# Kernel tuning notes

Measured on AMD Instinct MI355X. Metric: run time of the kernel, lower is better.

Reference implementation:

```python
import jax, jax.numpy as jnp
import numpy as np

N_OUT = 4096
N_IN = 4096
NNZ = 1600000
BATCH = 4096


def setup_inputs() -> dict:
    key = jax.random.key(0)
    k1, k2, k3, k4, k5 = jax.random.split(key, 5)
    inputs = jax.random.normal(k1, (N_IN, BATCH), dtype=jnp.float32)
    values = jax.random.normal(k2, (NNZ,), dtype=jnp.float32)
    biases = jax.random.normal(k3, (N_OUT, 1), dtype=jnp.float32)
    rows = jax.random.randint(k4, (NNZ,), 0, N_OUT, dtype=jnp.int32)
    cols = jax.random.randint(k5, (NNZ,), 0, N_IN, dtype=jnp.int32)
    return {"inputs": inputs, "values": values, "biases": biases,
            "rows": rows, "cols": cols}


def reference(inputs, values, biases, rows, cols):
    # torch.sparse.addmm(biases, W_sparse, inputs) with W COO [N_OUT, N_IN].
    # Scatter-add COO entries into a dense weight (duplicates summed, matching
    # coalesce semantics), then one dense GEMM -- avoids an [NNZ, BATCH]
    # gather intermediate while computing identical math.
    W = jnp.zeros((N_OUT, N_IN), dtype=values.dtype).at[rows, cols].add(values)
    out = W @ inputs + biases  # [N_OUT, BATCH], bias broadcast over columns
    return jax.nn.relu(out)    # activation epilogue
```

## Files before the change

### kernel.cpp

```cpp
#include <hip/hip_runtime.h>
#include <stdint.h>

#define N_OUT_  4096
#define N_IN_   4096
#define BATCH_  4096
#define NNZ_    1600000

typedef unsigned short ushort_t;
typedef float  f32x4  __attribute__((ext_vector_type(4)));
typedef short  short8 __attribute__((ext_vector_type(8)));
typedef __bf16 bf16x8 __attribute__((ext_vector_type(8)));

__device__ inline ushort_t f32_to_bf16(float f) {
  uint32_t u = __float_as_uint(f);
  uint32_t r = u + 0x7FFFu + ((u >> 16) & 1u);
  return (ushort_t)(r >> 16);
}
__device__ inline float bf16_to_f32(ushort_t h) {
  return __uint_as_float(((uint32_t)h) << 16);
}

__device__ inline void gload_lds16(const void* g, void* l) {
  __builtin_amdgcn_global_load_lds(
      (const __attribute__((address_space(1))) void*)g,
      (__attribute__((address_space(3))) void*)l,
      16, 0, 0);
}

__device__ inline f32x4 mfma_bf16(short8 a, short8 b, f32x4 c) {
  return __builtin_amdgcn_mfma_f32_16x16x32_bf16(
      __builtin_bit_cast(bf16x8, a), __builtin_bit_cast(bf16x8, b), c, 0, 0, 0);
}

#define BARRIER() asm volatile("s_barrier" ::: "memory")
template <int N> __device__ __forceinline__ void waitvm() {
  if constexpr (N == 8)      asm volatile("s_waitcnt vmcnt(8)" ::: "memory");
  else if constexpr (N == 6) asm volatile("s_waitcnt vmcnt(6)" ::: "memory");
  else if constexpr (N == 4) asm volatile("s_waitcnt vmcnt(4)" ::: "memory");
  else                       asm volatile("s_waitcnt vmcnt(0)" ::: "memory");
}

#define SC_BLOCKS2 3125
#define TR_TOTAL 4096
#define FUSED_BLOCKS 7294
#define HALF_NNZ 800000

__device__ inline void cas_add_bf16(uint32_t* __restrict__ W32, int i,
                                    const float* __restrict__ vals,
                                    const int* __restrict__ rows,
                                    const int* __restrict__ cols) {
  const size_t idx =
      (size_t)__builtin_nontemporal_load(rows + i) * N_IN_ +
      __builtin_nontemporal_load(cols + i);
  const float v = __builtin_nontemporal_load(vals + i);
  uint32_t* p = &W32[idx >> 1];
  const bool hi = (idx & 1) != 0;
  uint32_t cur = 0u;
  while (true) {
    ushort_t h = hi ? (ushort_t)(cur >> 16) : (ushort_t)(cur & 0xFFFFu);
    ushort_t nh = f32_to_bf16(bf16_to_f32(h) + v);
    uint32_t nw = hi ? ((cur & 0x0000FFFFu) | ((uint32_t)nh << 16))
                     : ((cur & 0xFFFF0000u) | (uint32_t)nh);
    uint32_t got = atomicCAS(p, cur, nw);
    if (got == cur) break;
    cur = got;
  }
}

__global__ __launch_bounds__(256) void scatter_transpose(
    const float* __restrict__ vals, const int* __restrict__ rows,
    const int* __restrict__ cols, uint32_t* __restrict__ W32,
    const float* __restrict__ in, ushort_t* __restrict__ out) {
  const int b = blockIdx.x;
  const int m = b % 7;
  if (m < 3) {
    const int sb = (b / 7) * 3 + m;
    if (sb >= SC_BLOCKS2) return;
    const int i = sb * 256 + threadIdx.x;
    cas_add_bf16(W32, i, vals, rows, cols);
    cas_add_bf16(W32, i + HALF_NNZ, vals, rows, cols);
  } else {
    const int tb = (b / 7) * 4 + (m - 3);
    if (tb >= TR_TOTAL) return;
    __shared__ float tile[64][65];
    const int bx = (tb & 63) * 64;
    const int by = (tb >> 6) * 64;
    const int t = threadIdx.x;
    const int lr = t >> 4;
    const int lc = (t & 15) * 4;
#pragma unroll
    for (int p = 0; p < 4; ++p) {
      const int i = lr + 16 * p;
      *(float4*)&tile[i][lc] =
          *(const float4*)&in[(size_t)(by + i) * BATCH_ + bx + lc];
    }
    __syncthreads();
    const int s = t & 7;
    const int j0 = t >> 3;
#pragma unroll
    for (int q = 0; q < 2; ++q) {
      const int j = j0 + 32 * q;
      uint32_t w0, w1, w2, w3;
      w0 = (uint32_t)f32_to_bf16(tile[8 * s + 0][j]) |
           ((uint32_t)f32_to_bf16(tile[8 * s + 1][j]) << 16);
      w1 = (uint32_t)f32_to_bf16(tile[8 * s + 2][j]) |
           ((uint32_t)f32_to_bf16(tile[8 * s + 3][j]) << 16);
      w2 = (uint32_t)f32_to_bf16(tile[8 * s + 4][j]) |
           ((uint32_t)f32_to_bf16(tile[8 * s + 5][j]) << 16);
      w3 = (uint32_t)f32_to_bf16(tile[8 * s + 6][j]) |
           ((uint32_t)f32_to_bf16(tile[8 * s + 7][j]) << 16);
      uint4 w = {w0, w1, w2, w3};
      *(uint4*)&out[(size_t)(bx + j) * N_IN_ + by + 8 * s] = w;
    }
  }
}

#define BM 256
#define BN 256
#define BK 32
#define KTILES 128
#define TILE_BYTES 32768
#define B_OFF 16384

__global__ __launch_bounds__(512, 2) void gemm_bias_relu(
    const ushort_t* __restrict__ A,
    const ushort_t* __restrict__ Bt,
    const float* __restrict__ bias,
    float* __restrict__ C) {
  __shared__ __align__(16) char smem[4 * TILE_BYTES];

  const int tid  = threadIdx.x;
  const int wid  = tid >> 6;
  const int lane = tid & 63;

  const int bid = blockIdx.x;
  const int swz = (bid & 7) * 32 + (bid >> 3);
  const int brow = (swz >> 4) * BM;
  const int bcol = (swz & 15) * BN;

  const int wr = wid >> 2;
  const int wc = wid & 3;
  const int fr = lane & 15;
  const int k0slot = lane >> 4;

  int aoff[8], boff[4];
#pragma unroll
  for (int mi = 0; mi < 8; ++mi) {
    int off = (wr * 128 + mi * 16 + fr) * 64 + k0slot * 16;
    aoff[mi] = off ^ (((off >> 7) & 3) << 4);
  }
#pragma unroll
  for (int ni = 0; ni < 4; ++ni) {
    int off = (wc * 64 + ni * 16 + fr) * 64 + k0slot * 16;
    boff[ni] = off ^ (((off >> 7) & 3) << 4);
  }

  const bool isB = wid >= 4;
  const int sw = isB ? wid - 4 : wid;
  const int swzl = lane ^ ((lane >> 3) & 3);
  const int rowInChunk = swzl >> 2;
  const int kelem = (swzl & 3) * 8;
  const ushort_t* gsrc = isB ? Bt : A;
  const size_t laneRowBase =
      (size_t)((isB ? bcol : brow) + sw * 64 + rowInChunk) * N_IN_ + kelem;
  const int ldsOpBase = isB ? B_OFF : 0;

#define STAGE(p, i, t)                                                        \
  gload_lds16(gsrc + laneRowBase + (size_t)(2 * (p) + (i)) * 16 * N_IN_ +     \
                  (size_t)(t) * BK,                                           \
              smem + ((t) & 3) * TILE_BYTES + ldsOpBase +                     \
                  (4 * sw + 2 * (p) + (i)) * 1024)

  f32x4 acc[8][4] = {};
  short8 aE[4], bE[4], aO[4], bO[4], aH[4];

#pragma unroll
  for (int t = 0; t < 3; ++t) {
    STAGE(0, 0, t); STAGE(0, 1, t); STAGE(1, 0, t); STAGE(1, 1, t);
  }
  waitvm<8>();
  BARRIER();
#pragma unroll
  for (int j = 0; j < 4; ++j) {
    aE[j] = *(const short8*)(smem + aoff[j]);
    bE[j] = *(const short8*)(smem + B_OFF + boff[j]);
  }

#define TILE(t, AL, BB, ALn, BBn, S_ON, VM, RA_ON)                            \
  do {                                                                        \
    const char* buf  = &smem[((t) & 3) * TILE_BYTES];                         \
    const char* bufn = &smem[(((t) + 1) & 3) * TILE_BYTES];                   \
    _Pragma("unroll") for (int j = 0; j < 4; ++j)                             \
        aH[j] = *(const short8*)(buf + aoff[j + 4]);                          \
    if (S_ON) { STAGE(0, 0, (t) + 3); STAGE(0, 1, (t) + 3); }                 \
    VM;                                                                       \
    BARRIER();                                                                \
    __builtin_amdgcn_s_setprio(1);                                            \
    _Pragma("unroll") for (int mi = 0; mi < 4; ++mi)                          \
        _Pragma("unroll") for (int ni = 0; ni < 4; ++ni)                      \
            acc[mi][ni] = mfma_bf16(AL[mi], BB[ni], acc[mi][ni]);             \
    __builtin_amdgcn_s_setprio(0);                                            \
    if (RA_ON) {                                                              \
      _Pragma("unroll") for (int j = 0; j < 4; ++j)                           \
          ALn[j] = *(const short8*)(bufn + aoff[j]);                          \
      _Pragma("unroll") for (int j = 0; j < 4; ++j)                           \
          BBn[j] = *(const short8*)(bufn + B_OFF + boff[j]);                  \
    }                                                                         \
    if (S_ON) { STAGE(1, 0, (t) + 3); STAGE(1, 1, (t) + 3); }                 \
    __builtin_amdgcn_s_setprio(1);                                            \
    _Pragma("unroll") for (int mi = 0; mi < 4; ++mi)                          \
        _Pragma("unroll") for (int ni = 0; ni < 4; ++ni)                      \
            acc[mi + 4][ni] = mfma_bf16(aH[mi], BB[ni], acc[mi + 4][ni]);     \
    __builtin_amdgcn_s_setprio(0);                                            \
    BARRIER();                                                                \
  } while (0)

  for (int t = 0; t < KTILES - 4; t += 2) {
    TILE(t,     aE, bE, aO, bO, 1, waitvm<6>(), 1);
    TILE(t + 1, aO, bO, aE, bE, 1, waitvm<6>(), 1);
  }
  TILE(KTILES - 4, aE, bE, aO, bO, 1, waitvm<6>(), 1);
  TILE(KTILES - 3, aO, bO, aE, bE, 0, waitvm<4>(), 1);
  TILE(KTILES - 2, aE, bE, aO, bO, 0, waitvm<0>(), 1);
  TILE(KTILES - 1, aO, bO, aE, bE, 0, (void)0,     0);

  const int r0 = brow + wr * 128 + k0slot * 4;
  const int c0 = bcol + wc * 64 + fr;
#pragma unroll
  for (int mi = 0; mi < 8; ++mi) {
#pragma unroll
    for (int r = 0; r < 4; ++r) {
      const int row = r0 + mi * 16 + r;
      const float b = bias[row];
#pragma unroll
      for (int ni = 0; ni < 4; ++ni) {
        float v = acc[mi][ni][r] + b;
        C[(size_t)row * BATCH_ + c0 + ni * 16] = v > 0.f ? v : 0.f;
      }
    }
  }
#undef TILE
#undef STAGE
}

extern "C" void kernel_launch(void* const* d_in, const int* in_sizes, int n_in,
                              void* d_out, int out_size, void* d_ws, size_t ws_size,
                              hipStream_t stream) {
  const float* inputs = (const float*)d_in[0];
  const float* values = (const float*)d_in[1];
  const float* biases = (const float*)d_in[2];
  const int*   rows   = (const int*)d_in[3];
  const int*   cols   = (const int*)d_in[4];
  float* out = (float*)d_out;

  const size_t W_BF16_BYTES = (size_t)N_OUT_ * N_IN_ * 2;
  if (ws_size < 2 * W_BF16_BYTES) return;
  char* ws = (char*)d_ws;
  ushort_t* Wb = (ushort_t*)ws;
  ushort_t* Bt = (ushort_t*)(ws + W_BF16_BYTES);

  hipMemsetAsync(Wb, 0, W_BF16_BYTES, stream);
  scatter_transpose<<<FUSED_BLOCKS, 256, 0, stream>>>(
      values, rows, cols, (uint32_t*)Wb, inputs, Bt);
  gemm_bias_relu<<<dim3(256), 512, 0, stream>>>(Wb, Bt, biases, out);
}
```

Measured before the change: 183.2 us.

## Replace register double-buffered LDS reads with per-half ping-pong schedule

The GEMM main loop stops prefetching the next tile's A/B fragments into a second register set during MFMAs. Each tile now loads B and the first half of A, waits on lgkmcnt, computes, then loads the second A half behind extra barriers. This lowers register pressure, which may allow higher occupancy. The cost is more barriers and exposed LDS latency, since fragment reads no longer overlap the previous tile's MFMAs.

```diff
diff --git a/kernel.cpp b/kernel.cpp
--- a/kernel.cpp
+++ b/kernel.cpp
@@ -33,6 +33,7 @@
 }
 
 #define BARRIER() asm volatile("s_barrier" ::: "memory")
+#define LGKM0()   asm volatile("s_waitcnt lgkmcnt(0)" ::: "memory")
 template <int N> __device__ __forceinline__ void waitvm() {
   if constexpr (N == 8)      asm volatile("s_waitcnt vmcnt(8)" ::: "memory");
   else if constexpr (N == 6) asm volatile("s_waitcnt vmcnt(6)" ::: "memory");
@@ -172,7 +173,7 @@
                   (4 * sw + 2 * (p) + (i)) * 1024)
 
   f32x4 acc[8][4] = {};
-  short8 aE[4], bE[4], aO[4], bO[4], aH[4];
+  short8 aF[4], bF[4];
 
 #pragma unroll
   for (int t = 0; t < 3; ++t) {
@@ -180,49 +181,43 @@
   }
   waitvm<8>();
   BARRIER();
-#pragma unroll
-  for (int j = 0; j < 4; ++j) {
-    aE[j] = *(const short8*)(smem + aoff[j]);
-    bE[j] = *(const short8*)(smem + B_OFF + boff[j]);
-  }
-
-#define TILE(t, AL, BB, ALn, BBn, S_ON, VM, RA_ON)                            \
+
+#define TILE(t, S_ON, VM)                                                     \
   do {                                                                        \
-    const char* buf  = &smem[((t) & 3) * TILE_BYTES];                         \
-    const char* bufn = &smem[(((t) + 1) & 3) * TILE_BYTES];                   \
+    const char* buf = &smem[((t) & 3) * TILE_BYTES];                          \
+                                                                 \
+    _Pragma("unroll") for (int ni = 0; ni < 4; ++ni)                          \
+        bF[ni] = *(const short8*)(buf + B_OFF + boff[ni]);                    \
     _Pragma("unroll") for (int j = 0; j < 4; ++j)                             \
-        aH[j] = *(const short8*)(buf + aoff[j + 4]);                          \
+        aF[j] = *(const short8*)(buf + aoff[j]);                              \
     if (S_ON) { STAGE(0, 0, (t) + 3); STAGE(0, 1, (t) + 3); }                 \
     VM;                                                                       \
     BARRIER();                                                                \
+    LGKM0();                                                                  \
     __builtin_amdgcn_s_setprio(1);                                            \
     _Pragma("unroll") for (int mi = 0; mi < 4; ++mi)                          \
         _Pragma("unroll") for (int ni = 0; ni < 4; ++ni)                      \
-            acc[mi][ni] = mfma_bf16(AL[mi], BB[ni], acc[mi][ni]);             \
+            acc[mi][ni] = mfma_bf16(aF[mi], bF[ni], acc[mi][ni]);             \
     __builtin_amdgcn_s_setprio(0);                                            \
-    if (RA_ON) {                                                              \
-      _Pragma("unroll") for (int j = 0; j < 4; ++j)                           \
-          ALn[j] = *(const short8*)(bufn + aoff[j]);                          \
-      _Pragma("unroll") for (int j = 0; j < 4; ++j)                           \
-          BBn[j] = *(const short8*)(bufn + B_OFF + boff[j]);                  \
-    }                                                                         \
+    BARRIER();                                                                \
+                                                                 \
+    _Pragma("unroll") for (int j = 0; j < 4; ++j)                             \
+        aF[j] = *(const short8*)(buf + aoff[j + 4]);                          \
     if (S_ON) { STAGE(1, 0, (t) + 3); STAGE(1, 1, (t) + 3); }                 \
+    BARRIER();                                                                \
+    LGKM0();                                                                  \
     __builtin_amdgcn_s_setprio(1);                                            \
     _Pragma("unroll") for (int mi = 0; mi < 4; ++mi)                          \
         _Pragma("unroll") for (int ni = 0; ni < 4; ++ni)                      \
-            acc[mi + 4][ni] = mfma_bf16(aH[mi], BB[ni], acc[mi + 4][ni]);     \
+            acc[mi + 4][ni] = mfma_bf16(aF[mi], bF[ni], acc[mi + 4][ni]);     \
     __builtin_amdgcn_s_setprio(0);                                            \
     BARRIER();                                                                \
   } while (0)
 
-  for (int t = 0; t < KTILES - 4; t += 2) {
-    TILE(t,     aE, bE, aO, bO, 1, waitvm<6>(), 1);
-    TILE(t + 1, aO, bO, aE, bE, 1, waitvm<6>(), 1);
-  }
-  TILE(KTILES - 4, aE, bE, aO, bO, 1, waitvm<6>(), 1);
-  TILE(KTILES - 3, aO, bO, aE, bE, 0, waitvm<4>(), 1);
-  TILE(KTILES - 2, aE, bE, aO, bO, 0, waitvm<0>(), 1);
-  TILE(KTILES - 1, aO, bO, aE, bE, 0, (void)0,     0);
+  for (int t = 0; t < KTILES - 3; ++t) TILE(t, 1, waitvm<6>());
+  TILE(KTILES - 3, 0, waitvm<4>());
+  TILE(KTILES - 2, 0, waitvm<0>());
+  TILE(KTILES - 1, 0, (void)0);
 
   const int r0 = brow + wr * 128 + k0slot * 4;
   const int c0 = bcol + wc * 64 + fr;
```

Measured after the change: 192.4 us. 1.05x slower.
